# Optimization experiments

Measured on AMD Instinct MI355X. Metric: run time of the kernel, lower is better.

Reference implementation:

```python
import jax, jax.numpy as jnp
import numpy as np
import math

D = 128
LAMBDA_INIT = 0.8 - 0.6 * math.exp(-0.3 * 1)  # depth=1


def _clin(xr, xi, wr, wi, br, bi):
    # complex linear: (xr + i xi) @ (wr + i wi)^T + (br + i bi)
    o_r = jnp.einsum('bhsd,od->bhso', xr, wr) - jnp.einsum('bhsd,od->bhso', xi, wi) + br
    o_i = jnp.einsum('bhsd,od->bhso', xr, wi) + jnp.einsum('bhsd,od->bhso', xi, wr) + bi
    return o_r, o_i


def setup_inputs() -> dict:
    key = jax.random.key(0)
    ks = jax.random.split(key, 32)
    B, H, S = 1, 12, 1024
    shp = (B, H, S, D)
    inp = {}
    names = ['q_r', 'q_i', 'k_r', 'k_i', 'v_r', 'v_i', 'pe_q_r', 'pe_q_i', 'pe_k_r', 'pe_k_i']
    for i, n in enumerate(names):
        inp[n] = jax.random.normal(ks[i], shp, dtype=jnp.float32)
    std = 1.0 / math.sqrt(D)
    inp['qw_r'] = jax.random.normal(ks[10], (2 * D, D), jnp.float32) * std
    inp['qw_i'] = jax.random.normal(ks[11], (2 * D, D), jnp.float32) * std
    inp['qb_r'] = jnp.zeros((2 * D,), jnp.float32)
    inp['qb_i'] = jnp.zeros((2 * D,), jnp.float32)
    for j, p in enumerate(['k', 'v', 'g', 'o']):
        inp[p + 'w_r'] = jax.random.normal(ks[12 + 2 * j], (D, D), jnp.float32) * std
        inp[p + 'w_i'] = jax.random.normal(ks[13 + 2 * j], (D, D), jnp.float32) * std
        inp[p + 'b_r'] = jnp.zeros((D,), jnp.float32)
        inp[p + 'b_i'] = jnp.zeros((D,), jnp.float32)
    inp['lq1'] = jax.random.normal(ks[20], (D,), jnp.float32) * 0.1
    inp['lk1'] = jax.random.normal(ks[21], (D,), jnp.float32) * 0.1
    inp['lq2'] = jax.random.normal(ks[22], (D,), jnp.float32) * 0.1
    inp['lk2'] = jax.random.normal(ks[23], (D,), jnp.float32) * 0.1
    inp['sub_w'] = jnp.ones((2 * D,), jnp.float32)
    return inp


def _forward(q_r, q_i, k_r, k_i, v_r, v_i, pe_q_r, pe_q_i, pe_k_r, pe_k_i,
             qw_r, qw_i, qb_r, qb_i, kw_r, kw_i, kb_r, kb_i,
             vw_r, vw_i, vb_r, vb_i, gw_r, gw_i, gb_r, gb_i,
             ow_r, ow_i, ob_r, ob_i, lq1, lk1, lq2, lk2, sub_w):
    scale = D ** (-0.5)
    qp_r, qp_i = _clin(q_r, q_i, qw_r, qw_i, qb_r, qb_i)   # [B,H,S,2D]
    kp_r, kp_i = _clin(k_r, k_i, kw_r, kw_i, kb_r, kb_i)   # [B,H,S,D]
    vp_r, vp_i = _clin(v_r, v_i, vw_r, vw_i, vb_r, vb_i)
    qp_r = qp_r + jnp.concatenate([pe_q_r, pe_q_r], axis=-1)
    qp_i = qp_i + jnp.concatenate([pe_q_i, pe_q_i], axis=-1)
    kp_r = kp_r + pe_k_r
    kp_i = kp_i + pe_k_i
    q1_r, q2_r = jnp.split(qp_r, 2, axis=-1)
    q1_i, q2_i = jnp.split(qp_i, 2, axis=-1)

    def attn_w(qr, qi):
        s_r = jnp.einsum('bhqd,bhkd->bhqk', qr, kp_r) + jnp.einsum('bhqd,bhkd->bhqk', qi, kp_i)
        s_i = jnp.einsum('bhqd,bhkd->bhqk', qi, kp_r) - jnp.einsum('bhqd,bhkd->bhqk', qr, kp_i)
        mag = jnp.sqrt(s_r ** 2 + s_i ** 2 + 1e-8) * scale
        return jax.nn.softmax(mag.astype(jnp.float32), axis=-1).astype(s_r.dtype)

    w1 = attn_w(q1_r, q1_i)
    w2 = attn_w(q2_r, q2_i)
    a1_r = jnp.einsum('bhqk,bhkd->bhqd', w1, vp_r)
    a1_i = jnp.einsum('bhqk,bhkd->bhqd', w1, vp_i)
    a2_r = jnp.einsum('bhqk,bhkd->bhqd', w2, vp_r)
    a2_i = jnp.einsum('bhqk,bhkd->bhqd', w2, vp_i)
    cat_r = jnp.concatenate([a1_r, a2_r], axis=-1)
    cat_i = jnp.concatenate([a1_i, a2_i], axis=-1)
    rms = jnp.sqrt(jnp.mean(cat_r ** 2 + cat_i ** 2, axis=-1, keepdims=True) + 1e-5)
    cat_r = cat_r / rms * sub_w
    cat_i = cat_i / rms * sub_w
    a1_r, a2_r = jnp.split(cat_r, 2, axis=-1)
    a1_i, a2_i = jnp.split(cat_i, 2, axis=-1)
    lam1 = jnp.exp(jnp.sum(lq1 * lk1))
    lam2 = jnp.exp(jnp.sum(lq2 * lk2))
    lam = jax.nn.sigmoid(lam1 - lam2 + LAMBDA_INIT)
    out_r = a1_r - lam * a2_r
    out_i = a1_i - lam * a2_i
    g_r, g_i = _clin(q_r, q_i, gw_r, gw_i, gb_r, gb_i)
    out_r, out_i = g_r * out_r - g_i * out_i, g_r * out_i + g_i * out_r
    out_r, out_i = _clin(out_r, out_i, ow_r, ow_i, ob_r, ob_i)
    return out_r, out_i


def reference(q_r, q_i, k_r, k_i, v_r, v_i, pe_q_r, pe_q_i, pe_k_r, pe_k_i,
              qw_r, qw_i, qb_r, qb_i, kw_r, kw_i, kb_r, kb_i,
              vw_r, vw_i, vb_r, vb_i, gw_r, gw_i, gb_r, gb_i,
              ow_r, ow_i, ob_r, ob_i, lq1, lk1, lq2, lk2, sub_w):
    return _forward(q_r, q_i, k_r, k_i, v_r, v_i, pe_q_r, pe_q_i, pe_k_r, pe_k_i,
                    qw_r, qw_i, qb_r, qb_i, kw_r, kw_i, kb_r, kb_i,
                    vw_r, vw_i, vb_r, vb_i, gw_r, gw_i, gb_r, gb_i,
                    ow_r, ow_i, ob_r, ob_i, lq1, lk1, lq2, lk2, sub_w)
```

## Files before the change

### kernel.cpp

```cpp
#include <hip/hip_runtime.h>
#include <math.h>

#define H 12
#define S 1024
#define D 128
#define NROWS (H * S)

typedef __attribute__((ext_vector_type(8))) _Float16 f16x8;
typedef __attribute__((ext_vector_type(4))) float f32x4;
typedef __attribute__((ext_vector_type(4))) int i32x4;

__device__ __forceinline__ short f2h(float f) {
    _Float16 h = (_Float16)f;
    return __builtin_bit_cast(short, h);
}
__device__ __forceinline__ float h2f(short s) {
    return (float)__builtin_bit_cast(_Float16, s);
}
__device__ __forceinline__ f16x8 fneg8(f16x8 v) {
    i32x4 u = __builtin_bit_cast(i32x4, v);
    u ^= (int)0x80008000;
    return __builtin_bit_cast(f16x8, u);
}

#define WS_QP_R   0ULL
#define WS_QP_I   6291456ULL
#define WS_KP_R   12582912ULL
#define WS_KP_I   15728640ULL
#define WS_VPT_R  18874368ULL
#define WS_VPT_I  22020096ULL
#define WS_GP_R   25165824ULL
#define WS_GP_I   28311552ULL
#define WS_ACAT_R 31457280ULL
#define WS_ACAT_I 37748736ULL
#define WS_LAM    44040192ULL
#define WS_SC     44040448ULL
#define W16_PER_HEAD   4194304ULL
#define STAT_PER_HEAD  16384ULL

__global__ void lam_kernel(const float* __restrict__ lq1, const float* __restrict__ lk1,
                           const float* __restrict__ lq2, const float* __restrict__ lk2,
                           float* __restrict__ lam_out)
{
    int t = threadIdx.x;
    float p1 = lq1[t] * lk1[t];
    float p2 = lq2[t] * lk2[t];
    #pragma unroll
    for (int off = 32; off; off >>= 1) {
        p1 += __shfl_xor(p1, off);
        p2 += __shfl_xor(p2, off);
    }
    __shared__ float s1[2], s2[2];
    if ((t & 63) == 0) { s1[t >> 6] = p1; s2[t >> 6] = p2; }
    __syncthreads();
    if (t == 0) {
        float l1 = expf(s1[0] + s1[1]);
        float l2 = expf(s2[0] + s2[1]);
        float x = l1 - l2 + 0.3555090675909693f;
        lam_out[0] = 1.0f / (1.0f + expf(-x));
    }
}

__global__ __launch_bounds__(256) void proj_all(
    const float* __restrict__ q_r, const float* __restrict__ q_i,
    const float* __restrict__ k_r, const float* __restrict__ k_i,
    const float* __restrict__ v_r, const float* __restrict__ v_i,
    const float* __restrict__ pe_q_r, const float* __restrict__ pe_q_i,
    const float* __restrict__ pe_k_r, const float* __restrict__ pe_k_i,
    const float* __restrict__ qw_r, const float* __restrict__ qw_i,
    const float* __restrict__ qb_r, const float* __restrict__ qb_i,
    const float* __restrict__ kw_r, const float* __restrict__ kw_i,
    const float* __restrict__ kb_r, const float* __restrict__ kb_i,
    const float* __restrict__ vw_r, const float* __restrict__ vw_i,
    const float* __restrict__ vb_r, const float* __restrict__ vb_i,
    const float* __restrict__ gw_r, const float* __restrict__ gw_i,
    const float* __restrict__ gb_r, const float* __restrict__ gb_i,
    short* __restrict__ qp_r, short* __restrict__ qp_i,
    short* __restrict__ kp_r, short* __restrict__ kp_i,
    short* __restrict__ vpT_r, short* __restrict__ vpT_i,
    short* __restrict__ gp_r, short* __restrict__ gp_i)
{
    const int y = blockIdx.y;
    const float *xr, *xi, *wr, *wi, *br, *bi, *per = nullptr, *pei = nullptr;
    short *outr_, *outi_;
    int M, omode, col0;
    if (y < 4)      { xr = q_r; xi = q_i; wr = qw_r; wi = qw_i; br = qb_r; bi = qb_i;
                      per = pe_q_r; pei = pe_q_i; outr_ = qp_r; outi_ = qp_i;
                      M = 256; omode = 1; col0 = y * 64; }
    else if (y < 6) { xr = k_r; xi = k_i; wr = kw_r; wi = kw_i; br = kb_r; bi = kb_i;
                      per = pe_k_r; pei = pe_k_i; outr_ = kp_r; outi_ = kp_i;
                      M = 128; omode = 1; col0 = (y - 4) * 64; }
    else if (y < 8) { xr = v_r; xi = v_i; wr = vw_r; wi = vw_i; br = vb_r; bi = vb_i;
                      outr_ = vpT_r; outi_ = vpT_i;
                      M = 128; omode = 2; col0 = (y - 6) * 64; }
    else            { xr = q_r; xi = q_i; wr = gw_r; wi = gw_i; br = gb_r; bi = gb_i;
                      outr_ = gp_r; outi_ = gp_i;
                      M = 128; omode = 1; col0 = (y - 8) * 64; }

    __shared__ short As[64 * 72], Brs[64 * 72], Bis[64 * 72];
    const int t = threadIdx.x;
    const int row0 = blockIdx.x * 64;
    const int lane = t & 63, wid = t >> 6;
    const int wm = (wid >> 1) * 32, wn = (wid & 1) * 32;
    const int fm = lane & 15, fq = lane >> 4;
    f32x4 zero4 = {0.f, 0.f, 0.f, 0.f};
    f32x4 accr[2][2], acci[2][2];
    #pragma unroll
    for (int i = 0; i < 2; ++i)
        #pragma unroll
        for (int j = 0; j < 2; ++j) { accr[i][j] = zero4; acci[i][j] = zero4; }

    for (int c = 0; c < 4; ++c) {
        const bool hi = (c >= 2);
        const int kb = (c & 1) * 64;
        const float* Asrc = hi ? xi : xr;
        const float* Brsrc = hi ? wi : wr;
        const float* Bisrc = hi ? wr : wi;
        const float bsign = hi ? -1.0f : 1.0f;
        __syncthreads();
        #pragma unroll
        for (int it = 0; it < 4; ++it) {
            int lin = it * 256 + t;
            int r = lin >> 4, k4 = (lin & 15) * 4;
            float4 va = *(const float4*)&Asrc[(size_t)(row0 + r) * 128 + kb + k4];
            *(short4*)&As[r * 72 + k4] = make_short4(f2h(va.x), f2h(va.y), f2h(va.z), f2h(va.w));
            float4 vr = *(const float4*)&Brsrc[(size_t)(col0 + r) * 128 + kb + k4];
            *(short4*)&Brs[r * 72 + k4] = make_short4(f2h(bsign * vr.x), f2h(bsign * vr.y),
                                                      f2h(bsign * vr.z), f2h(bsign * vr.w));
            float4 vi = *(const float4*)&Bisrc[(size_t)(col0 + r) * 128 + kb + k4];
            *(short4*)&Bis[r * 72 + k4] = make_short4(f2h(vi.x), f2h(vi.y), f2h(vi.z), f2h(vi.w));
        }
        __syncthreads();
        #pragma unroll
        for (int ks = 0; ks < 64; ks += 32) {
            f16x8 bfr[2], bfi[2];
            #pragma unroll
            for (int j = 0; j < 2; ++j) {
                bfr[j] = *(const f16x8*)&Brs[(wn + j * 16 + fm) * 72 + ks + fq * 8];
                bfi[j] = *(const f16x8*)&Bis[(wn + j * 16 + fm) * 72 + ks + fq * 8];
            }
            #pragma unroll
            for (int i = 0; i < 2; ++i) {
                f16x8 a = *(const f16x8*)&As[(wm + i * 16 + fm) * 72 + ks + fq * 8];
                #pragma unroll
                for (int j = 0; j < 2; ++j) {
                    accr[i][j] = __builtin_amdgcn_mfma_f32_16x16x32_f16(a, bfr[j], accr[i][j], 0, 0, 0);
                    acci[i][j] = __builtin_amdgcn_mfma_f32_16x16x32_f16(a, bfi[j], acci[i][j], 0, 0, 0);
                }
            }
        }
    }
    #pragma unroll
    for (int i = 0; i < 2; ++i)
        #pragma unroll
        for (int j = 0; j < 2; ++j) {
            int colc = col0 + wn + j * 16 + fm;
            float bbr = br[colc], bbi = bi[colc];
            if (omode == 2) {
                int rb = row0 + wm + i * 16 + fq * 4;
                int hq = rb >> 10, sq = rb & 1023;
                short4 o_r4 = make_short4(f2h(accr[i][j][0] + bbr), f2h(accr[i][j][1] + bbr),
                                          f2h(accr[i][j][2] + bbr), f2h(accr[i][j][3] + bbr));
                short4 o_i4 = make_short4(f2h(acci[i][j][0] + bbi), f2h(acci[i][j][1] + bbi),
                                          f2h(acci[i][j][2] + bbi), f2h(acci[i][j][3] + bbi));
                size_t ob = ((size_t)(hq * 128 + colc)) * 1024 + sq;
                *(short4*)&outr_[ob] = o_r4;
                *(short4*)&outi_[ob] = o_i4;
            } else {
                #pragma unroll
                for (int reg = 0; reg < 4; ++reg) {
                    int rr = row0 + wm + i * 16 + fq * 4 + reg;
                    float o_r = accr[i][j][reg] + bbr;
                    float o_i = acci[i][j][reg] + bbi;
                    if (per) {
                        o_r += per[(size_t)rr * 128 + (colc & 127)];
                        o_i += pei[(size_t)rr * 128 + (colc & 127)];
                    }
                    outr_[(size_t)rr * M + colc] = f2h(o_r);
                    outi_[(size_t)rr * M + colc] = f2h(o_i);
                }
            }
        }
}

__global__ __launch_bounds__(256) void oproj_mfma(
    const short* __restrict__ gp_r, const short* __restrict__ gp_i,
    const float* __restrict__ wr, const float* __restrict__ wi,
    const float* __restrict__ br, const float* __restrict__ bi,
    float* __restrict__ outr, float* __restrict__ outi)
{
    __shared__ short As[64 * 72], Brs[64 * 72], Bis[64 * 72];
    const int t = threadIdx.x;
    const int row0 = blockIdx.x * 64, col0 = blockIdx.y * 64;
    const int lane = t & 63, wid = t >> 6;
    const int wm = (wid >> 1) * 32, wn = (wid & 1) * 32;
    const int fm = lane & 15, fq = lane >> 4;
    f32x4 zero4 = {0.f, 0.f, 0.f, 0.f};
    f32x4 accr[2][2], acci[2][2];
    #pragma unroll
    for (int i = 0; i < 2; ++i)
        #pragma unroll
        for (int j = 0; j < 2; ++j) { accr[i][j] = zero4; acci[i][j] = zero4; }

    for (int c = 0; c < 4; ++c) {
        const bool hi = (c >= 2);
        const int kb = (c & 1) * 64;
        const short* Asrc = hi ? gp_i : gp_r;
        const float* Brsrc = hi ? wi : wr;
        const float* Bisrc = hi ? wr : wi;
        const float bsign = hi ? -1.0f : 1.0f;
        __syncthreads();
        #pragma unroll
        for (int it = 0; it < 4; ++it) {
            int lin = it * 256 + t;
            int r = lin >> 4, k4 = (lin & 15) * 4;
            *(short4*)&As[r * 72 + k4] = *(const short4*)&Asrc[(size_t)(row0 + r) * 128 + kb + k4];
            float4 vr = *(const float4*)&Brsrc[(size_t)(col0 + r) * 128 + kb + k4];
            *(short4*)&Brs[r * 72 + k4] = make_short4(f2h(bsign * vr.x), f2h(bsign * vr.y),
                                                      f2h(bsign * vr.z), f2h(bsign * vr.w));
            float4 vi = *(const float4*)&Bisrc[(size_t)(col0 + r) * 128 + kb + k4];
            *(short4*)&Bis[r * 72 + k4] = make_short4(f2h(vi.x), f2h(vi.y), f2h(vi.z), f2h(vi.w));
        }
        __syncthreads();
        #pragma unroll
        for (int ks = 0; ks < 64; ks += 32) {
            f16x8 bfr[2], bfi[2];
            #pragma unroll
            for (int j = 0; j < 2; ++j) {
                bfr[j] = *(const f16x8*)&Brs[(wn + j * 16 + fm) * 72 + ks + fq * 8];
                bfi[j] = *(const f16x8*)&Bis[(wn + j * 16 + fm) * 72 + ks + fq * 8];
            }
            #pragma unroll
            for (int i = 0; i < 2; ++i) {
                f16x8 a = *(const f16x8*)&As[(wm + i * 16 + fm) * 72 + ks + fq * 8];
                #pragma unroll
                for (int j = 0; j < 2; ++j) {
                    accr[i][j] = __builtin_amdgcn_mfma_f32_16x16x32_f16(a, bfr[j], accr[i][j], 0, 0, 0);
                    acci[i][j] = __builtin_amdgcn_mfma_f32_16x16x32_f16(a, bfi[j], acci[i][j], 0, 0, 0);
                }
            }
        }
    }
    #pragma unroll
    for (int i = 0; i < 2; ++i)
        #pragma unroll
        for (int j = 0; j < 2; ++j) {
            int colc = col0 + wn + j * 16 + fm;
            float bbr = br[colc], bbi = bi[colc];
            #pragma unroll
            for (int reg = 0; reg < 4; ++reg) {
                int rr = row0 + wm + i * 16 + fq * 4 + reg;
                outr[(size_t)rr * 128 + colc] = accr[i][j][reg] + bbr;
                outi[(size_t)rr * 128 + colc] = acci[i][j][reg] + bbi;
            }
        }
}

__global__ __launch_bounds__(256) void score_mfma(
    const short* __restrict__ qp_r, const short* __restrict__ qp_i,
    const short* __restrict__ kp_r, const short* __restrict__ kp_i,
    short* __restrict__ w16, int h0)
{
    __shared__ short Qr[64 * 72], Qi[64 * 72], Kt[128 * 72];
    const int t = threadIdx.x;
    const int hh = blockIdx.z >> 1, map = blockIdx.z & 1;
    const int h = h0 + hh;
    const int q0 = blockIdx.x * 64, c0 = blockIdx.y * 128;
    const int lane = t & 63, wid = t >> 6;
    const int wm = (wid >> 1) * 32, wn = (wid & 1) * 64;
    const int fm = lane & 15, fq = lane >> 4;
    f32x4 zero4 = {0.f, 0.f, 0.f, 0.f};
    f32x4 sr[2][4], si[2][4];
    #pragma unroll
    for (int i = 0; i < 2; ++i)
        #pragma unroll
        for (int j = 0; j < 4; ++j) { sr[i][j] = zero4; si[i][j] = zero4; }

    for (int kb = 0; kb < 2; ++kb) {
        const int kbase = map * 128 + kb * 64;
        __syncthreads();
        #pragma unroll
        for (int i = 0; i < 4; ++i) {
            int lin = i * 256 + t;
            int r = lin >> 4, k4 = (lin & 15) * 4;
            size_t qb = (size_t)(h * S + q0 + r) * 256 + kbase + k4;
            *(short4*)&Qr[r * 72 + k4] = *(const short4*)&qp_r[qb];
            *(short4*)&Qi[r * 72 + k4] = *(const short4*)&qp_i[qb];
        }
        #pragma unroll
        for (int i = 0; i < 8; ++i) {
            int lin = i * 256 + t;
            int r = lin >> 4, k4 = (lin & 15) * 4;
            *(short4*)&Kt[r * 72 + k4] =
                *(const short4*)&kp_r[(size_t)(h * S + c0 + r) * 128 + kb * 64 + k4];
        }
        __syncthreads();
        f16x8 aR[2][2], aI[2][2];
        #pragma unroll
        for (int ks = 0; ks < 2; ++ks)
            #pragma unroll
            for (int i = 0; i < 2; ++i) {
                int ao = (wm + i * 16 + fm) * 72 + ks * 32 + fq * 8;
                aR[ks][i] = *(const f16x8*)&Qr[ao];
                aI[ks][i] = *(const f16x8*)&Qi[ao];
            }
        #pragma unroll
        for (int ks = 0; ks < 2; ++ks) {
            f16x8 b[4];
            #pragma unroll
            for (int j = 0; j < 4; ++j)
                b[j] = *(const f16x8*)&Kt[(wn + j * 16 + fm) * 72 + ks * 32 + fq * 8];
            #pragma unroll
            for (int i = 0; i < 2; ++i)
                #pragma unroll
                for (int j = 0; j < 4; ++j) {
                    sr[i][j] = __builtin_amdgcn_mfma_f32_16x16x32_f16(aR[ks][i], b[j], sr[i][j], 0, 0, 0);
                    si[i][j] = __builtin_amdgcn_mfma_f32_16x16x32_f16(aI[ks][i], b[j], si[i][j], 0, 0, 0);
                }
        }
        __syncthreads();
        #pragma unroll
        for (int i = 0; i < 8; ++i) {
            int lin = i * 256 + t;
            int r = lin >> 4, k4 = (lin & 15) * 4;
            *(short4*)&Kt[r * 72 + k4] =
                *(const short4*)&kp_i[(size_t)(h * S + c0 + r) * 128 + kb * 64 + k4];
        }
        __syncthreads();
        #pragma unroll
        for (int ks = 0; ks < 2; ++ks) {
            f16x8 b[4];
            #pragma unroll
            for (int j = 0; j < 4; ++j)
                b[j] = *(const f16x8*)&Kt[(wn + j * 16 + fm) * 72 + ks * 32 + fq * 8];
            f16x8 nR0 = fneg8(aR[ks][0]), nR1 = fneg8(aR[ks][1]);
            #pragma unroll
            for (int j = 0; j < 4; ++j) {
                sr[0][j] = __builtin_amdgcn_mfma_f32_16x16x32_f16(aI[ks][0], b[j], sr[0][j], 0, 0, 0);
                si[0][j] = __builtin_amdgcn_mfma_f32_16x16x32_f16(nR0, b[j], si[0][j], 0, 0, 0);
                sr[1][j] = __builtin_amdgcn_mfma_f32_16x16x32_f16(aI[ks][1], b[j], sr[1][j], 0, 0, 0);
                si[1][j] = __builtin_amdgcn_mfma_f32_16x16x32_f16(nR1, b[j], si[1][j], 0, 0, 0);
            }
        }
    }
    const float scale = 0.08838834764831845f;
    #pragma unroll
    for (int i = 0; i < 2; ++i)
        #pragma unroll
        for (int j = 0; j < 4; ++j) {
            int kcol = c0 + wn + j * 16 + fm;
            #pragma unroll
            for (int reg = 0; reg < 4; ++reg) {
                int q = q0 + wm + i * 16 + fq * 4 + reg;
                float r1 = sr[i][j][reg], I1 = si[i][j][reg];
                float m1 = sqrtf(fmaf(r1, r1, fmaf(I1, I1, 1e-8f))) * scale;
                w16[(((size_t)hh * 2 + map) * S + q) * S + kcol] = f2h(m1);
            }
        }
}

__global__ __launch_bounds__(256) void smstats(const short* __restrict__ w16,
                                               float2* __restrict__ stats)
{
    const short* row = w16 + (size_t)blockIdx.x * S;
    int t = threadIdx.x;
    short4 s = ((const short4*)row)[t];
    float f0 = h2f(s.x), f1 = h2f(s.y), f2v = h2f(s.z), f3 = h2f(s.w);
    float m = fmaxf(fmaxf(f0, f1), fmaxf(f2v, f3));
    #pragma unroll
    for (int off = 32; off; off >>= 1) m = fmaxf(m, __shfl_xor(m, off));
    __shared__ float redm[4], reds[4];
    int w = t >> 6;
    if ((t & 63) == 0) redm[w] = m;
    __syncthreads();
    m = fmaxf(fmaxf(redm[0], redm[1]), fmaxf(redm[2], redm[3]));
    float ssum = __expf(f0 - m) + __expf(f1 - m) + __expf(f2v - m) + __expf(f3 - m);
    #pragma unroll
    for (int off = 32; off; off >>= 1) ssum += __shfl_xor(ssum, off);
    if ((t & 63) == 0) reds[w] = ssum;
    __syncthreads();
    if (t == 0) {
        float total = reds[0] + reds[1] + reds[2] + reds[3];
        stats[blockIdx.x] = make_float2(m, 1.0f / total);
    }
}

__global__ __launch_bounds__(256) void av_mfma(
    const short* __restrict__ w16, const float2* __restrict__ stats,
    const short* __restrict__ vpT_r, const short* __restrict__ vpT_i,
    short* __restrict__ acat_r, short* __restrict__ acat_i, int h0)
{
    __shared__ short W1[32 * 72], W2[32 * 72], Vc[128 * 72];
    const int t = threadIdx.x;
    const int hh = blockIdx.z, h = h0 + hh;
    const int comp = blockIdx.y;
    const int q0 = blockIdx.x * 32;
    const short* vpT = comp ? vpT_i : vpT_r;
    short* acat = comp ? acat_i : acat_r;
    const float2* st1 = stats + ((size_t)hh * 2 + 0) * S;
    const float2* st2 = stats + ((size_t)hh * 2 + 1) * S;
    const int lane = t & 63, wid = t >> 6;
    const int wm = (wid >> 1) * 16, wn = (wid & 1) * 64;
    const int fm = lane & 15, fq = lane >> 4;
    f32x4 zero4 = {0.f, 0.f, 0.f, 0.f};
    f32x4 a1[4], a2[4];
    #pragma unroll
    for (int j = 0; j < 4; ++j) { a1[j] = zero4; a2[j] = zero4; }

    for (int k0 = 0; k0 < S; k0 += 64) {
        __syncthreads();
        #pragma unroll
        for (int it = 0; it < 2; ++it) {
            int lin = it * 256 + t;
            int r = lin >> 4, k4 = (lin & 15) * 4;
            float2 s1v = st1[q0 + r];
            float2 s2v = st2[q0 + r];
            short4 m1 = *(const short4*)&w16[(((size_t)hh * 2 + 0) * S + q0 + r) * S + k0 + k4];
            short4 m2 = *(const short4*)&w16[(((size_t)hh * 2 + 1) * S + q0 + r) * S + k0 + k4];
            *(short4*)&W1[r * 72 + k4] = make_short4(
                f2h(__expf(h2f(m1.x) - s1v.x) * s1v.y), f2h(__expf(h2f(m1.y) - s1v.x) * s1v.y),
                f2h(__expf(h2f(m1.z) - s1v.x) * s1v.y), f2h(__expf(h2f(m1.w) - s1v.x) * s1v.y));
            *(short4*)&W2[r * 72 + k4] = make_short4(
                f2h(__expf(h2f(m2.x) - s2v.x) * s2v.y), f2h(__expf(h2f(m2.y) - s2v.x) * s2v.y),
                f2h(__expf(h2f(m2.z) - s2v.x) * s2v.y), f2h(__expf(h2f(m2.w) - s2v.x) * s2v.y));
        }
        #pragma unroll
        for (int it = 0; it < 8; ++it) {
            int lin = it * 256 + t;
            int dd = lin >> 4, k4 = (lin & 15) * 4;
            *(short4*)&Vc[dd * 72 + k4] = *(const short4*)&vpT[(size_t)(h * 128 + dd) * 1024 + k0 + k4];
        }
        __syncthreads();
        #pragma unroll
        for (int ks = 0; ks < 64; ks += 32) {
            f16x8 b[4];
            #pragma unroll
            for (int j = 0; j < 4; ++j)
                b[j] = *(const f16x8*)&Vc[(wn + j * 16 + fm) * 72 + ks + fq * 8];
            int wo = (wm + fm) * 72 + ks + fq * 8;
            f16x8 w1f = *(const f16x8*)&W1[wo];
            f16x8 w2f = *(const f16x8*)&W2[wo];
            #pragma unroll
            for (int j = 0; j < 4; ++j) {
                a1[j] = __builtin_amdgcn_mfma_f32_16x16x32_f16(w1f, b[j], a1[j], 0, 0, 0);
                a2[j] = __builtin_amdgcn_mfma_f32_16x16x32_f16(w2f, b[j], a2[j], 0, 0, 0);
            }
        }
    }
    #pragma unroll
    for (int j = 0; j < 4; ++j) {
        int d = wn + j * 16 + fm;
        #pragma unroll
        for (int reg = 0; reg < 4; ++reg) {
            int q = q0 + wm + fq * 4 + reg;
            size_t rowb = (size_t)(h * S + q) * 256;
            acat[rowb + d]       = f2h(a1[j][reg]);
            acat[rowb + 128 + d] = f2h(a2[j][reg]);
        }
    }
}

__global__ __launch_bounds__(256) void rmsgate_kernel(
    const short* __restrict__ acat_r, const short* __restrict__ acat_i,
    const float* __restrict__ sub_w, const float* __restrict__ lam_ptr,
    short* __restrict__ gp_r, short* __restrict__ gp_i)
{
    int row = blockIdx.x;
    int t = threadIdx.x;
    float ar = h2f(acat_r[(size_t)row * 256 + t]);
    float ai = h2f(acat_i[(size_t)row * 256 + t]);
    float ss = fmaf(ar, ar, ai * ai);
    #pragma unroll
    for (int off = 32; off; off >>= 1) ss += __shfl_xor(ss, off);
    __shared__ float red[4];
    if ((t & 63) == 0) red[t >> 6] = ss;
    __syncthreads();
    float total = red[0] + red[1] + red[2] + red[3];
    float inv_rms = 1.0f / sqrtf(total * (1.0f / 256.0f) + 1e-5f);
    float sw = sub_w[t];
    __shared__ float Cr[256], Ci[256];
    Cr[t] = ar * inv_rms * sw;
    Ci[t] = ai * inv_rms * sw;
    __syncthreads();
    if (t < 128) {
        float lam = lam_ptr[0];
        float o_r = Cr[t] - lam * Cr[t + 128];
        float o_i = Ci[t] - lam * Ci[t + 128];
        float gr = h2f(gp_r[(size_t)row * 128 + t]);
        float gi = h2f(gp_i[(size_t)row * 128 + t]);
        gp_r[(size_t)row * 128 + t] = f2h(gr * o_r - gi * o_i);
        gp_i[(size_t)row * 128 + t] = f2h(gr * o_i + gi * o_r);
    }
}

extern "C" void kernel_launch(void* const* d_in, const int* in_sizes, int n_in,
                              void* d_out, int out_size, void* d_ws, size_t ws_size,
                              hipStream_t stream)
{
    (void)in_sizes; (void)n_in; (void)out_size;
    const float* q_r    = (const float*)d_in[0];
    const float* q_i    = (const float*)d_in[1];
    const float* k_r    = (const float*)d_in[2];
    const float* k_i    = (const float*)d_in[3];
    const float* v_r    = (const float*)d_in[4];
    const float* v_i    = (const float*)d_in[5];
    const float* pe_q_r = (const float*)d_in[6];
    const float* pe_q_i = (const float*)d_in[7];
    const float* pe_k_r = (const float*)d_in[8];
    const float* pe_k_i = (const float*)d_in[9];
    const float* qw_r   = (const float*)d_in[10];
    const float* qw_i   = (const float*)d_in[11];
    const float* qb_r   = (const float*)d_in[12];
    const float* qb_i   = (const float*)d_in[13];
    const float* kw_r   = (const float*)d_in[14];
    const float* kw_i   = (const float*)d_in[15];
    const float* kb_r   = (const float*)d_in[16];
    const float* kb_i   = (const float*)d_in[17];
    const float* vw_r   = (const float*)d_in[18];
    const float* vw_i   = (const float*)d_in[19];
    const float* vb_r   = (const float*)d_in[20];
    const float* vb_i   = (const float*)d_in[21];
    const float* gw_r   = (const float*)d_in[22];
    const float* gw_i   = (const float*)d_in[23];
    const float* gb_r   = (const float*)d_in[24];
    const float* gb_i   = (const float*)d_in[25];
    const float* ow_r   = (const float*)d_in[26];
    const float* ow_i   = (const float*)d_in[27];
    const float* ob_r   = (const float*)d_in[28];
    const float* ob_i   = (const float*)d_in[29];
    const float* lq1    = (const float*)d_in[30];
    const float* lk1    = (const float*)d_in[31];
    const float* lq2    = (const float*)d_in[32];
    const float* lk2    = (const float*)d_in[33];
    const float* sub_w  = (const float*)d_in[34];

    char* ws = (char*)d_ws;
    short* qp_r   = (short*)(ws + WS_QP_R);
    short* qp_i   = (short*)(ws + WS_QP_I);
    short* kp_r   = (short*)(ws + WS_KP_R);
    short* kp_i   = (short*)(ws + WS_KP_I);
    short* vpT_r  = (short*)(ws + WS_VPT_R);
    short* vpT_i  = (short*)(ws + WS_VPT_I);
    short* gp_r   = (short*)(ws + WS_GP_R);
    short* gp_i   = (short*)(ws + WS_GP_I);
    short* acat_r = (short*)(ws + WS_ACAT_R);
    short* acat_i = (short*)(ws + WS_ACAT_I);
    float* lam    = (float*)(ws + WS_LAM);
    short* w16    = (short*)(ws + WS_SC);

    float* out_r = (float*)d_out;
    float* out_i = out_r + (size_t)NROWS * D;

    size_t avail = ws_size > WS_SC ? ws_size - WS_SC : 0;
    int nh_chunk = (int)(avail / (W16_PER_HEAD + STAT_PER_HEAD));
    if (nh_chunk < 1) nh_chunk = 1;
    if (nh_chunk > H) nh_chunk = H;
    float2* stats = (float2*)(ws + WS_SC + (size_t)nh_chunk * W16_PER_HEAD);

    lam_kernel<<<1, 128, 0, stream>>>(lq1, lk1, lq2, lk2, lam);

    proj_all<<<dim3(192, 10), 256, 0, stream>>>(
        q_r, q_i, k_r, k_i, v_r, v_i, pe_q_r, pe_q_i, pe_k_r, pe_k_i,
        qw_r, qw_i, qb_r, qb_i, kw_r, kw_i, kb_r, kb_i,
        vw_r, vw_i, vb_r, vb_i, gw_r, gw_i, gb_r, gb_i,
        qp_r, qp_i, kp_r, kp_i, vpT_r, vpT_i, gp_r, gp_i);

    for (int h0 = 0; h0 < H; h0 += nh_chunk) {
        int nhh = (H - h0 < nh_chunk) ? (H - h0) : nh_chunk;
        score_mfma<<<dim3(16, 8, nhh * 2), 256, 0, stream>>>(qp_r, qp_i, kp_r, kp_i, w16, h0);
        smstats<<<nhh * 2 * S, 256, 0, stream>>>(w16, stats);
        av_mfma<<<dim3(32, 2, nhh), 256, 0, stream>>>(w16, stats, vpT_r, vpT_i, acat_r, acat_i, h0);
    }

    rmsgate_kernel<<<NROWS, 256, 0, stream>>>(acat_r, acat_i, sub_w, lam, gp_r, gp_i);

    oproj_mfma<<<dim3(192, 2), 256, 0, stream>>>(gp_r, gp_i, ow_r, ow_i, ob_r, ob_i, out_r, out_i);
}
```

Measured before the change: 296.7 us.

## Fold lambda into rmsgate, halve oproj tile rows, two rows per smstats block

Removes the separate lambda kernel and recomputes the lambda scalar inside every rmsgate block, saving one launch at the cost of redundant per-row reductions and exps. The output projection tile shrinks from 64 to 32 rows, doubling the grid for more parallelism while reloading the weight tiles twice as often. smstats now handles two score rows per block using 16-byte loads, halving its block count.

After: 300.3 us. About the same (+1.2%).

```diff
diff --git a/kernel.cpp b/kernel.cpp
--- a/kernel.cpp
+++ b/kernel.cpp
@@ -33,33 +33,9 @@
 #define WS_GP_I   28311552ULL
 #define WS_ACAT_R 31457280ULL
 #define WS_ACAT_I 37748736ULL
-#define WS_LAM    44040192ULL
 #define WS_SC     44040448ULL
 #define W16_PER_HEAD   4194304ULL
 #define STAT_PER_HEAD  16384ULL
-
-__global__ void lam_kernel(const float* __restrict__ lq1, const float* __restrict__ lk1,
-                           const float* __restrict__ lq2, const float* __restrict__ lk2,
-                           float* __restrict__ lam_out)
-{
-    int t = threadIdx.x;
-    float p1 = lq1[t] * lk1[t];
-    float p2 = lq2[t] * lk2[t];
-    #pragma unroll
-    for (int off = 32; off; off >>= 1) {
-        p1 += __shfl_xor(p1, off);
-        p2 += __shfl_xor(p2, off);
-    }
-    __shared__ float s1[2], s2[2];
-    if ((t & 63) == 0) { s1[t >> 6] = p1; s2[t >> 6] = p2; }
-    __syncthreads();
-    if (t == 0) {
-        float l1 = expf(s1[0] + s1[1]);
-        float l2 = expf(s2[0] + s2[1]);
-        float x = l1 - l2 + 0.3555090675909693f;
-        lam_out[0] = 1.0f / (1.0f + expf(-x));
-    }
-}
 
 __global__ __launch_bounds__(256) void proj_all(
     const float* __restrict__ q_r, const float* __restrict__ q_i,
@@ -189,18 +165,16 @@
     const float* __restrict__ br, const float* __restrict__ bi,
     float* __restrict__ outr, float* __restrict__ outi)
 {
-    __shared__ short As[64 * 72], Brs[64 * 72], Bis[64 * 72];
+    __shared__ short As[32 * 72], Brs[64 * 72], Bis[64 * 72];
     const int t = threadIdx.x;
-    const int row0 = blockIdx.x * 64, col0 = blockIdx.y * 64;
+    const int row0 = blockIdx.x * 32, col0 = blockIdx.y * 64;
     const int lane = t & 63, wid = t >> 6;
-    const int wm = (wid >> 1) * 32, wn = (wid & 1) * 32;
+    const int wm = (wid >> 1) * 16, wn = (wid & 1) * 32;
     const int fm = lane & 15, fq = lane >> 4;
     f32x4 zero4 = {0.f, 0.f, 0.f, 0.f};
-    f32x4 accr[2][2], acci[2][2];
-    #pragma unroll
-    for (int i = 0; i < 2; ++i)
-        #pragma unroll
-        for (int j = 0; j < 2; ++j) { accr[i][j] = zero4; acci[i][j] = zero4; }
+    f32x4 accr[2], acci[2];
+    #pragma unroll
+    for (int j = 0; j < 2; ++j) { accr[j] = zero4; acci[j] = zero4; }
 
     for (int c = 0; c < 4; ++c) {
         const bool hi = (c >= 2);
@@ -211,10 +185,15 @@
         const float bsign = hi ? -1.0f : 1.0f;
         __syncthreads();
         #pragma unroll
+        for (int it = 0; it < 2; ++it) {
+            int lin = it * 256 + t;
+            int r = lin >> 4, k4 = (lin & 15) * 4;
+            *(short4*)&As[r * 72 + k4] = *(const short4*)&Asrc[(size_t)(row0 + r) * 128 + kb + k4];
+        }
+        #pragma unroll
         for (int it = 0; it < 4; ++it) {
             int lin = it * 256 + t;
             int r = lin >> 4, k4 = (lin & 15) * 4;
-            *(short4*)&As[r * 72 + k4] = *(const short4*)&Asrc[(size_t)(row0 + r) * 128 + kb + k4];
             float4 vr = *(const float4*)&Brsrc[(size_t)(col0 + r) * 128 + kb + k4];
             *(short4*)&Brs[r * 72 + k4] = make_short4(f2h(bsign * vr.x), f2h(bsign * vr.y),
                                                       f2h(bsign * vr.z), f2h(bsign * vr.w));
@@ -230,30 +209,25 @@
                 bfr[j] = *(const f16x8*)&Brs[(wn + j * 16 + fm) * 72 + ks + fq * 8];
                 bfi[j] = *(const f16x8*)&Bis[(wn + j * 16 + fm) * 72 + ks + fq * 8];
             }
-            #pragma unroll
-            for (int i = 0; i < 2; ++i) {
-                f16x8 a = *(const f16x8*)&As[(wm + i * 16 + fm) * 72 + ks + fq * 8];
-                #pragma unroll
-                for (int j = 0; j < 2; ++j) {
-                    accr[i][j] = __builtin_amdgcn_mfma_f32_16x16x32_f16(a, bfr[j], accr[i][j], 0, 0, 0);
-                    acci[i][j] = __builtin_amdgcn_mfma_f32_16x16x32_f16(a, bfi[j], acci[i][j], 0, 0, 0);
-                }
-            }
-        }
-    }
-    #pragma unroll
-    for (int i = 0; i < 2; ++i)
-        #pragma unroll
-        for (int j = 0; j < 2; ++j) {
-            int colc = col0 + wn + j * 16 + fm;
-            float bbr = br[colc], bbi = bi[colc];
-            #pragma unroll
-            for (int reg = 0; reg < 4; ++reg) {
-                int rr = row0 + wm + i * 16 + fq * 4 + reg;
-                outr[(size_t)rr * 128 + colc] = accr[i][j][reg] + bbr;
-                outi[(size_t)rr * 128 + colc] = acci[i][j][reg] + bbi;
-            }
-        }
+            f16x8 a = *(const f16x8*)&As[(wm + fm) * 72 + ks + fq * 8];
+            #pragma unroll
+            for (int j = 0; j < 2; ++j) {
+                accr[j] = __builtin_amdgcn_mfma_f32_16x16x32_f16(a, bfr[j], accr[j], 0, 0, 0);
+                acci[j] = __builtin_amdgcn_mfma_f32_16x16x32_f16(a, bfi[j], acci[j], 0, 0, 0);
+            }
+        }
+    }
+    #pragma unroll
+    for (int j = 0; j < 2; ++j) {
+        int colc = col0 + wn + j * 16 + fm;
+        float bbr = br[colc], bbi = bi[colc];
+        #pragma unroll
+        for (int reg = 0; reg < 4; ++reg) {
+            int rr = row0 + wm + fq * 4 + reg;
+            outr[(size_t)rr * 128 + colc] = accr[j][reg] + bbr;
+            outi[(size_t)rr * 128 + colc] = acci[j][reg] + bbi;
+        }
+    }
 }
 
 __global__ __launch_bounds__(256) void score_mfma(
@@ -362,26 +336,37 @@
 __global__ __launch_bounds__(256) void smstats(const short* __restrict__ w16,
                                                float2* __restrict__ stats)
 {
-    const short* row = w16 + (size_t)blockIdx.x * S;
     int t = threadIdx.x;
-    short4 s = ((const short4*)row)[t];
-    float f0 = h2f(s.x), f1 = h2f(s.y), f2v = h2f(s.z), f3 = h2f(s.w);
-    float m = fmaxf(fmaxf(f0, f1), fmaxf(f2v, f3));
+    int rl = t >> 7;
+    int row = blockIdx.x * 2 + rl;
+    int li = t & 127;
+    const short* rp = w16 + (size_t)row * S;
+    i32x4 v = *(const i32x4*)&rp[li * 8];
+    short s8[8];
+    *(i32x4*)s8 = v;
+    float f[8];
+    #pragma unroll
+    for (int j = 0; j < 8; ++j) f[j] = h2f(s8[j]);
+    float m = f[0];
+    #pragma unroll
+    for (int j = 1; j < 8; ++j) m = fmaxf(m, f[j]);
     #pragma unroll
     for (int off = 32; off; off >>= 1) m = fmaxf(m, __shfl_xor(m, off));
     __shared__ float redm[4], reds[4];
     int w = t >> 6;
     if ((t & 63) == 0) redm[w] = m;
     __syncthreads();
-    m = fmaxf(fmaxf(redm[0], redm[1]), fmaxf(redm[2], redm[3]));
-    float ssum = __expf(f0 - m) + __expf(f1 - m) + __expf(f2v - m) + __expf(f3 - m);
+    m = fmaxf(redm[rl * 2], redm[rl * 2 + 1]);
+    float ssum = 0.f;
+    #pragma unroll
+    for (int j = 0; j < 8; ++j) ssum += __expf(f[j] - m);
     #pragma unroll
     for (int off = 32; off; off >>= 1) ssum += __shfl_xor(ssum, off);
     if ((t & 63) == 0) reds[w] = ssum;
     __syncthreads();
-    if (t == 0) {
-        float total = reds[0] + reds[1] + reds[2] + reds[3];
-        stats[blockIdx.x] = make_float2(m, 1.0f / total);
+    if ((t & 127) == 0) {
+        float total = reds[rl * 2] + reds[rl * 2 + 1];
+        stats[row] = make_float2(m, 1.0f / total);
     }
 }
 
@@ -462,7 +447,9 @@
 
 __global__ __launch_bounds__(256) void rmsgate_kernel(
     const short* __restrict__ acat_r, const short* __restrict__ acat_i,
-    const float* __restrict__ sub_w, const float* __restrict__ lam_ptr,
+    const float* __restrict__ sub_w,
+    const float* __restrict__ lq1, const float* __restrict__ lk1,
+    const float* __restrict__ lq2, const float* __restrict__ lk2,
     short* __restrict__ gp_r, short* __restrict__ gp_i)
 {
     int row = blockIdx.x;
@@ -470,12 +457,22 @@
     float ar = h2f(acat_r[(size_t)row * 256 + t]);
     float ai = h2f(acat_i[(size_t)row * 256 + t]);
     float ss = fmaf(ar, ar, ai * ai);
-    #pragma unroll
-    for (int off = 32; off; off >>= 1) ss += __shfl_xor(ss, off);
-    __shared__ float red[4];
-    if ((t & 63) == 0) red[t >> 6] = ss;
+    float p1 = (t < 128) ? lq1[t] * lk1[t] : 0.f;
+    float p2 = (t < 128) ? lq2[t] * lk2[t] : 0.f;
+    #pragma unroll
+    for (int off = 32; off; off >>= 1) {
+        ss += __shfl_xor(ss, off);
+        p1 += __shfl_xor(p1, off);
+        p2 += __shfl_xor(p2, off);
+    }
+    __shared__ float red[4], r1s[4], r2s[4];
+    if ((t & 63) == 0) { red[t >> 6] = ss; r1s[t >> 6] = p1; r2s[t >> 6] = p2; }
     __syncthreads();
     float total = red[0] + red[1] + red[2] + red[3];
+    float s1 = r1s[0] + r1s[1] + r1s[2] + r1s[3];
+    float s2 = r2s[0] + r2s[1] + r2s[2] + r2s[3];
+    float xlam = expf(s1) - expf(s2) + 0.3555090675909693f;
+    float lam = 1.0f / (1.0f + expf(-xlam));
     float inv_rms = 1.0f / sqrtf(total * (1.0f / 256.0f) + 1e-5f);
     float sw = sub_w[t];
     __shared__ float Cr[256], Ci[256];
@@ -483,7 +480,6 @@
     Ci[t] = ai * inv_rms * sw;
     __syncthreads();
     if (t < 128) {
-        float lam = lam_ptr[0];
         float o_r = Cr[t] - lam * Cr[t + 128];
         float o_i = Ci[t] - lam * Ci[t + 128];
         float gr = h2f(gp_r[(size_t)row * 128 + t]);
@@ -545,7 +541,6 @@
     short* gp_i   = (short*)(ws + WS_GP_I);
     short* acat_r = (short*)(ws + WS_ACAT_R);
     short* acat_i = (short*)(ws + WS_ACAT_I);
-    float* lam    = (float*)(ws + WS_LAM);
     short* w16    = (short*)(ws + WS_SC);
 
     float* out_r = (float*)d_out;
@@ -557,8 +552,6 @@
     if (nh_chunk > H) nh_chunk = H;
     float2* stats = (float2*)(ws + WS_SC + (size_t)nh_chunk * W16_PER_HEAD);
 
-    lam_kernel<<<1, 128, 0, stream>>>(lq1, lk1, lq2, lk2, lam);
-
     proj_all<<<dim3(192, 10), 256, 0, stream>>>(
         q_r, q_i, k_r, k_i, v_r, v_i, pe_q_r, pe_q_i, pe_k_r, pe_k_i,
         qw_r, qw_i, qb_r, qb_i, kw_r, kw_i, kb_r, kb_i,
@@ -568,11 +561,12 @@
     for (int h0 = 0; h0 < H; h0 += nh_chunk) {
         int nhh = (H - h0 < nh_chunk) ? (H - h0) : nh_chunk;
         score_mfma<<<dim3(16, 8, nhh * 2), 256, 0, stream>>>(qp_r, qp_i, kp_r, kp_i, w16, h0);
-        smstats<<<nhh * 2 * S, 256, 0, stream>>>(w16, stats);
+        smstats<<<nhh * S, 256, 0, stream>>>(w16, stats);
         av_mfma<<<dim3(32, 2, nhh), 256, 0, stream>>>(w16, stats, vpT_r, vpT_i, acat_r, acat_i, h0);
     }
 
-    rmsgate_kernel<<<NROWS, 256, 0, stream>>>(acat_r, acat_i, sub_w, lam, gp_r, gp_i);
-
-    oproj_mfma<<<dim3(192, 2), 256, 0, stream>>>(gp_r, gp_i, ow_r, ow_i, ob_r, ob_i, out_r, out_i);
-}
+    rmsgate_kernel<<<NROWS, 256, 0, stream>>>(acat_r, acat_i, sub_w,
+                                              lq1, lk1, lq2, lk2, gp_r, gp_i);
+
+    oproj_mfma<<<dim3(384, 2), 256, 0, stream>>>(gp_r, gp_i, ow_r, ow_i, ob_r, ob_i, out_r, out_i);
+}
```
